# Performance work log

Measured on AMD Instinct MI355X. Metric: run time of the kernel, lower is better.

The kernel has to match this reference:

```python
import jax, jax.numpy as jnp
import numpy as np

B, N, D = 4, 1024, 512
H, DH = 8, 64
TC, AB = 512, 16
EPS = 1e-5
NEG = 1e6


def setup_inputs() -> dict:
    key = jax.random.key(0)
    ks = jax.random.split(key, 10)
    inp = {
        "x": jax.random.normal(ks[0], (B, N, D), jnp.float32),
        "time": jax.random.normal(ks[1], (B, 1, TC), jnp.float32),
        "attn_bias": jax.random.normal(ks[2], (B, AB, N, N), jnp.float32),
        "seq_mask": jnp.ones((B, N), jnp.float32),
        "gamma": jnp.ones((D,), jnp.float32),
        "Wt": jax.random.normal(ks[3], (2 * D, TC), jnp.float32) * 0.02,
        "bt": jnp.zeros((2 * D,), jnp.float32),
        "Wq": jax.random.normal(ks[4], (H * DH, D), jnp.float32) * 0.02,
        "Wkv": jax.random.normal(ks[5], (2 * H * DH, D), jnp.float32) * 0.02,
        "Wo": jax.random.normal(ks[6], (D, H * DH), jnp.float32) * 0.02,
        "Wb": jax.random.normal(ks[7], (H, AB), jnp.float32) * 0.02,
        "bb": jnp.zeros((H,), jnp.float32),
    }
    return inp


def reference(x, time, attn_bias, seq_mask, gamma, Wt, bt, Wq, Wkv, Wo, Wb, bb):
    # context defaults to raw x BEFORE norm/FiLM/mask (faithful to source order)
    ctx = x
    # LayerNorm (beta buffer is zero)
    mu = jnp.mean(x, axis=-1, keepdims=True)
    var = jnp.mean(jnp.square(x - mu), axis=-1, keepdims=True)
    xn = (x - mu) * jax.lax.rsqrt(var + EPS) * gamma
    # FiLM time conditioning: SiLU -> Linear -> chunk
    t = jax.nn.silu(time) @ Wt.T + bt            # [B,1,2D]
    scale, shift = jnp.split(t, 2, axis=-1)
    xn = xn * (scale + 1.0) + shift
    # seq mask on queries' input
    xn = xn * seq_mask[..., None]
    # projections
    q = xn @ Wq.T                                 # [B,N,H*DH]
    kv = ctx @ Wkv.T                              # [B,N,2*H*DH]
    k, v = jnp.split(kv, 2, axis=-1)
    to_heads = lambda t: t.reshape(B, N, H, DH).transpose(0, 2, 1, 3)
    q, k, v = to_heads(q), to_heads(k), to_heads(v)
    q = q * (DH ** -0.5)
    sim = jnp.einsum('bhid,bhjd->bhij', q, k)     # [B,H,N,N]
    # learned projection of attn_bias channels -> heads
    bias = jnp.einsum('baij,ha->bhij', attn_bias, Wb) + bb[None, :, None, None]
    sim = sim + bias
    m = seq_mask[:, None, :, None] * seq_mask[:, None, None, :]  # [B,1,N,N]
    sim = sim - (1.0 - m) * NEG
    attn = jax.nn.softmax(sim, axis=-1)
    out = jnp.einsum('bhij,bhjd->bhid', attn, v)
    out = out.transpose(0, 2, 1, 3).reshape(B, N, H * DH)
    out = out @ Wo.T
    return out * seq_mask[..., None]
```

## Files before the change

kernel.cpp:

```cpp
#include <hip/hip_runtime.h>
#include <hip/hip_bf16.h>
#include <math.h>

#define B_  4
#define N_  1024
#define D_  512
#define H_  8
#define DH_ 64
#define TC_ 512
#define AB_ 16
#define EPS_ 1e-5f
#define NEG_ 1e6f

typedef _Float16 half8v __attribute__((ext_vector_type(8)));
typedef _Float16 half4v __attribute__((ext_vector_type(4)));
typedef float floatx4 __attribute__((ext_vector_type(4)));

__global__ void film_kernel(const float* __restrict__ time_in,
                            const float* __restrict__ Wt,
                            const float* __restrict__ bt,
                            float* __restrict__ film) {
    int idx = blockIdx.x * blockDim.x + threadIdx.x;
    int b = idx >> 10;
    int c = idx & 1023;
    const float* trow = time_in + b * TC_;
    const float* wrow = Wt + (size_t)c * TC_;
    float acc = bt[c];
    for (int j = 0; j < TC_; ++j) {
        float tv = trow[j];
        float s = tv / (1.f + __expf(-tv));
        acc += s * wrow[j];
    }
    film[idx] = acc;
}

__global__ __launch_bounds__(256)
void cvt_f16_kernel(const float* __restrict__ in, _Float16* __restrict__ out,
                    int n4) {
    int i = blockIdx.x * blockDim.x + threadIdx.x;
    if (i < n4) {
        float4 v = ((const float4*)in)[i];
        half4v o;
        o.x = (_Float16)v.x; o.y = (_Float16)v.y;
        o.z = (_Float16)v.z; o.w = (_Float16)v.w;
        ((half4v*)out)[i] = o;
    }
}

__global__ __launch_bounds__(256)
void ln_film_kernel(const float* __restrict__ x,
                    const float* __restrict__ gamma,
                    const float* __restrict__ film,
                    const float* __restrict__ seq_mask,
                    _Float16* __restrict__ xnh) {
    int row = blockIdx.x;
    int b = row >> 10;
    int t = threadIdx.x;
    const float* xr = x + (size_t)row * D_;
    float v0 = xr[t];
    float v1 = xr[t + 256];
    float s = v0 + v1;
    float sq = v0 * v0 + v1 * v1;
    int lane = t & 63, wave = t >> 6;
    #pragma unroll
    for (int off = 32; off; off >>= 1) {
        s  += __shfl_down(s, off);
        sq += __shfl_down(sq, off);
    }
    __shared__ float rs[4], rq[4];
    if (lane == 0) { rs[wave] = s; rq[wave] = sq; }
    __syncthreads();
    float mu  = (rs[0] + rs[1] + rs[2] + rs[3]) * (1.f / D_);
    float ex2 = (rq[0] + rq[1] + rq[2] + rq[3]) * (1.f / D_);
    float var = ex2 - mu * mu;
    float rstd = rsqrtf(var + EPS_);
    float mrow = seq_mask[row];
    const float* scale = film + (size_t)b * 2 * D_;
    const float* shift = scale + D_;
    {
        int d = t;
        float val = (v0 - mu) * rstd * gamma[d];
        val = val * (scale[d] + 1.f) + shift[d];
        xnh[(size_t)row * D_ + d] = (_Float16)(val * mrow);
    }
    {
        int d = t + 256;
        float val = (v1 - mu) * rstd * gamma[d];
        val = val * (scale[d] + 1.f) + shift[d];
        xnh[(size_t)row * D_ + d] = (_Float16)(val * mrow);
    }
}

#define LDK 40
__global__ __launch_bounds__(256)
void gemm_mfma_f16(const _Float16* __restrict__ A,
                   const _Float16* __restrict__ Bt,
                   float* __restrict__ C,
                   int M, int Nn, int K) {
    __shared__ _Float16 As[128 * LDK];
    __shared__ _Float16 Bs[128 * LDK];
    int t = threadIdx.x;
    int wave = t >> 6, lane = t & 63;
    int quad = lane >> 4, l16 = lane & 15;
    int m0 = blockIdx.y * 128, n0 = blockIdx.x * 128;
    int wm = (wave >> 1) * 64, wn = (wave & 1) * 64;

    floatx4 acc[4][4];
    #pragma unroll
    for (int i = 0; i < 4; ++i)
        #pragma unroll
        for (int j = 0; j < 4; ++j)
            acc[i][j] = (floatx4){0.f, 0.f, 0.f, 0.f};

    int row0 = t >> 2;
    int seg0 = (t & 3) * 8;

    for (int k0 = 0; k0 < K; k0 += 32) {
        half8v a0 = *(const half8v*)(A  + (size_t)(m0 + row0)      * K + k0 + seg0);
        half8v a1 = *(const half8v*)(A  + (size_t)(m0 + row0 + 64) * K + k0 + seg0);
        half8v b0 = *(const half8v*)(Bt + (size_t)(n0 + row0)      * K + k0 + seg0);
        half8v b1 = *(const half8v*)(Bt + (size_t)(n0 + row0 + 64) * K + k0 + seg0);
        __syncthreads();
        *(half8v*)(As + row0 * LDK + seg0)        = a0;
        *(half8v*)(As + (row0 + 64) * LDK + seg0) = a1;
        *(half8v*)(Bs + row0 * LDK + seg0)        = b0;
        *(half8v*)(Bs + (row0 + 64) * LDK + seg0) = b1;
        __syncthreads();

        half8v af[4], bf[4];
        #pragma unroll
        for (int i = 0; i < 4; ++i)
            af[i] = *(half8v*)(As + (wm + i * 16 + l16) * LDK + quad * 8);
        #pragma unroll
        for (int j = 0; j < 4; ++j)
            bf[j] = *(half8v*)(Bs + (wn + j * 16 + l16) * LDK + quad * 8);
        #pragma unroll
        for (int i = 0; i < 4; ++i)
            #pragma unroll
            for (int j = 0; j < 4; ++j)
                acc[i][j] = __builtin_amdgcn_mfma_f32_16x16x32_f16(
                    af[i], bf[j], acc[i][j], 0, 0, 0);
    }

    #pragma unroll
    for (int i = 0; i < 4; ++i)
        #pragma unroll
        for (int j = 0; j < 4; ++j)
            #pragma unroll
            for (int r = 0; r < 4; ++r) {
                int grow = m0 + wm + i * 16 + quad * 4 + r;
                int gcol = n0 + wn + j * 16 + l16;
                C[(size_t)grow * Nn + gcol] = acc[i][j][r];
            }
}

__global__ __launch_bounds__(256)
void bias_proj_kernel(const float* __restrict__ ab,
                      const float* __restrict__ seq_mask,
                      const float* __restrict__ Wb,
                      const float* __restrict__ bb,
                      __hip_bfloat16* __restrict__ pb) {
    __shared__ float wbs[8][16];
    __shared__ float bbs[8];
    int blk = blockIdx.x;
    int b = blk >> 10;
    int i = blk & 1023;
    int t = threadIdx.x;
    if (t < 128) wbs[t >> 4][t & 15] = Wb[t];
    if (t < 8)   bbs[t] = bb[t];
    __syncthreads();

    float accx[8], accy[8], accz[8], accw[8];
    #pragma unroll
    for (int h = 0; h < 8; ++h) { accx[h] = accy[h] = accz[h] = accw[h] = bbs[h]; }

    const float* base = ab + ((size_t)(b * AB_) * N_ + i) * N_ + t * 4;
    #pragma unroll
    for (int a = 0; a < AB_; ++a) {
        float4 v = *(const float4*)(base + (size_t)a * N_ * N_);
        #pragma unroll
        for (int h = 0; h < 8; ++h) {
            float w = wbs[h][a];
            accx[h] += v.x * w;
            accy[h] += v.y * w;
            accz[h] += v.z * w;
            accw[h] += v.w * w;
        }
    }
    float mq = seq_mask[blk];
    float4 mk = *(const float4*)(seq_mask + b * N_ + t * 4);
    float px = (1.f - mq * mk.x) * NEG_;
    float py = (1.f - mq * mk.y) * NEG_;
    float pz = (1.f - mq * mk.z) * NEG_;
    float pw = (1.f - mq * mk.w) * NEG_;

    #pragma unroll
    for (int h = 0; h < 8; ++h) {
        __hip_bfloat16 tmp[4];
        tmp[0] = __float2bfloat16(accx[h] - px);
        tmp[1] = __float2bfloat16(accy[h] - py);
        tmp[2] = __float2bfloat16(accz[h] - pz);
        tmp[3] = __float2bfloat16(accw[h] - pw);
        size_t off = (((size_t)(b * 8 + h) * N_) + i) * N_ + t * 4;
        *(ushort4*)(pb + off) = *(ushort4*)tmp;
    }
}

#define LDF 72
#define LDP 72
#define LDV 68
__global__ __launch_bounds__(256, 4)
void flash_mfma_kernel(const float* __restrict__ q,
                       const float* __restrict__ kv,
                       const __hip_bfloat16* __restrict__ pb,
                       const float* __restrict__ seq_mask,
                       _Float16* __restrict__ atth) {
    __shared__ _Float16 Qs[64 * LDF];
    __shared__ _Float16 Ks[64 * LDF];
    __shared__ _Float16 Ps[64 * LDP];
    __shared__ _Float16 Vt[64 * LDV];

    int z  = blockIdx.x;
    int qt = z & 15;
    int h  = (z >> 4) & 7;
    int b  = z >> 7;
    int i0 = qt * 64;
    int t  = threadIdx.x;
    int wave = t >> 6, lane = t & 63;
    int quad = lane >> 4, l16 = lane & 15;
    int strip = wave * 16;

    const float* qbase = q + ((size_t)(b * N_ + i0)) * 512 + h * 64;
    #pragma unroll
    for (int l = 0; l < 4; ++l) {
        int idx = l * 256 + t;
        int r = idx >> 4, c4 = (idx & 15) * 4;
        float4 v = *(const float4*)(qbase + (size_t)r * 512 + c4);
        half4v o;
        o.x = (_Float16)(v.x * 0.125f);
        o.y = (_Float16)(v.y * 0.125f);
        o.z = (_Float16)(v.z * 0.125f);
        o.w = (_Float16)(v.w * 0.125f);
        *(half4v*)&Qs[r * LDF + c4] = o;
    }
    __syncthreads();
    half8v qf[2];
    qf[0] = *(half8v*)&Qs[(strip + l16) * LDF + quad * 8];
    qf[1] = *(half8v*)&Qs[(strip + l16) * LDF + 32 + quad * 8];

    float m_r[4], l_r[4];
    floatx4 acco[4];
    #pragma unroll
    for (int r = 0; r < 4; ++r) { m_r[r] = -1e30f; l_r[r] = 0.f; }
    #pragma unroll
    for (int tile = 0; tile < 4; ++tile)
        acco[tile] = (floatx4){0.f, 0.f, 0.f, 0.f};

    const float* kvbase = kv + (size_t)b * N_ * 1024 + h * 64;
    const __hip_bfloat16* pbb =
        pb + ((size_t)((b * 8 + h) * N_) + i0 + strip + quad * 4) * N_;

    for (int jt = 0; jt < 16; ++jt) {
        int j0 = jt * 64;
        float4 kreg[4], vreg[4];
        #pragma unroll
        for (int l = 0; l < 4; ++l) {
            int idx = l * 256 + t;
            int r = idx >> 4, c4 = (idx & 15) * 4;
            const float* p = kvbase + (size_t)(j0 + r) * 1024 + c4;
            kreg[l] = *(const float4*)p;
            vreg[l] = *(const float4*)(p + 512);
        }
        floatx4 accs[4];
        #pragma unroll
        for (int tile = 0; tile < 4; ++tile)
            #pragma unroll
            for (int r = 0; r < 4; ++r)
                accs[tile][r] = __bfloat162float(
                    pbb[(size_t)r * N_ + j0 + tile * 16 + l16]);

        __syncthreads();
        #pragma unroll
        for (int l = 0; l < 4; ++l) {
            int idx = l * 256 + t;
            int r = idx >> 4, c4 = (idx & 15) * 4;
            half4v kh;
            kh.x = (_Float16)kreg[l].x;
            kh.y = (_Float16)kreg[l].y;
            kh.z = (_Float16)kreg[l].z;
            kh.w = (_Float16)kreg[l].w;
            *(half4v*)&Ks[r * LDF + c4] = kh;
            Vt[(c4 + 0) * LDV + r] = (_Float16)vreg[l].x;
            Vt[(c4 + 1) * LDV + r] = (_Float16)vreg[l].y;
            Vt[(c4 + 2) * LDV + r] = (_Float16)vreg[l].z;
            Vt[(c4 + 3) * LDV + r] = (_Float16)vreg[l].w;
        }
        __syncthreads();

        #pragma unroll
        for (int c = 0; c < 2; ++c)
            #pragma unroll
            for (int tile = 0; tile < 4; ++tile) {
                half8v kf = *(half8v*)&Ks[(tile * 16 + l16) * LDF + c * 32 + quad * 8];
                accs[tile] = __builtin_amdgcn_mfma_f32_16x16x32_f16(
                    qf[c], kf, accs[tile], 0, 0, 0);
            }

        float rm[4];
        #pragma unroll
        for (int r = 0; r < 4; ++r)
            rm[r] = fmaxf(fmaxf(accs[0][r], accs[1][r]),
                          fmaxf(accs[2][r], accs[3][r]));
        #pragma unroll
        for (int off = 1; off < 16; off <<= 1)
            #pragma unroll
            for (int r = 0; r < 4; ++r)
                rm[r] = fmaxf(rm[r], __shfl_xor(rm[r], off));
        float alpha[4], rsum[4], pv[4][4];
        #pragma unroll
        for (int r = 0; r < 4; ++r) {
            float mn = fmaxf(m_r[r], rm[r]);
            alpha[r] = __expf(m_r[r] - mn);
            m_r[r] = mn;
            float s = 0.f;
            #pragma unroll
            for (int tile = 0; tile < 4; ++tile) {
                float e = __expf(accs[tile][r] - mn);
                pv[tile][r] = e;
                s += e;
            }
            rsum[r] = s;
        }
        #pragma unroll
        for (int off = 1; off < 16; off <<= 1)
            #pragma unroll
            for (int r = 0; r < 4; ++r)
                rsum[r] += __shfl_xor(rsum[r], off);
        #pragma unroll
        for (int r = 0; r < 4; ++r) {
            l_r[r] = l_r[r] * alpha[r] + rsum[r];
            #pragma unroll
            for (int tile = 0; tile < 4; ++tile) {
                acco[tile][r] *= alpha[r];
                Ps[(strip + quad * 4 + r) * LDP + tile * 16 + l16] =
                    (_Float16)pv[tile][r];
            }
        }
        __syncthreads();

        #pragma unroll
        for (int c = 0; c < 2; ++c) {
            half8v pf = *(half8v*)&Ps[(strip + l16) * LDP + c * 32 + quad * 8];
            #pragma unroll
            for (int tile = 0; tile < 4; ++tile) {
                union { half8v v8; half4v v4[2]; } vu;
                int vbase = (tile * 16 + l16) * LDV + c * 32 + quad * 8;
                vu.v4[0] = *(half4v*)&Vt[vbase];
                vu.v4[1] = *(half4v*)&Vt[vbase + 4];
                acco[tile] = __builtin_amdgcn_mfma_f32_16x16x32_f16(
                    pf, vu.v8, acco[tile], 0, 0, 0);
            }
        }
    }

    #pragma unroll
    for (int r = 0; r < 4; ++r) {
        int row = i0 + strip + quad * 4 + r;
        float msk = seq_mask[b * N_ + row];
        float inv = msk / l_r[r];
        _Float16* ob = atth + ((size_t)(b * N_ + row)) * 512 + h * 64;
        #pragma unroll
        for (int tile = 0; tile < 4; ++tile)
            ob[tile * 16 + l16] = (_Float16)(acco[tile][r] * inv);
    }
}

extern "C" void kernel_launch(void* const* d_in, const int* in_sizes, int n_in,
                              void* d_out, int out_size, void* d_ws, size_t ws_size,
                              hipStream_t stream) {
    const float* x         = (const float*)d_in[0];
    const float* time_in   = (const float*)d_in[1];
    const float* attn_bias = (const float*)d_in[2];
    const float* seq_mask  = (const float*)d_in[3];
    const float* gamma     = (const float*)d_in[4];
    const float* Wt        = (const float*)d_in[5];
    const float* bt        = (const float*)d_in[6];
    const float* Wq        = (const float*)d_in[7];
    const float* Wkv       = (const float*)d_in[8];
    const float* Wo        = (const float*)d_in[9];
    const float* Wb        = (const float*)d_in[10];
    const float* bb        = (const float*)d_in[11];
    float* out = (float*)d_out;

    char* ws = (char*)d_ws;
    const size_t KB = 1024, MB = 1024 * 1024;
    float*     film = (float*)ws;
    _Float16*  xnh  = (_Float16*)(ws + 16 * KB);
    _Float16*  xh   = (_Float16*)(ws + 16 * KB + 4 * MB);
    _Float16*  Wqh  = (_Float16*)(ws + 16 * KB + 8 * MB);
    _Float16*  Wkvh = (_Float16*)(ws + 16 * KB + 8 * MB + 512 * KB);
    _Float16*  Woh  = (_Float16*)(ws + 16 * KB + 9 * MB + 512 * KB);
    float*     qb   = (float*)(ws + 16 * KB + 10 * MB);
    float*     kvb  = (float*)(ws + 16 * KB + 18 * MB);
    _Float16*  atth = (_Float16*)(ws + 16 * KB + 34 * MB);
    __hip_bfloat16* pb = (__hip_bfloat16*)(ws + 16 * KB + 38 * MB);

    film_kernel<<<16, 256, 0, stream>>>(time_in, Wt, bt, film);
    ln_film_kernel<<<4096, 256, 0, stream>>>(x, gamma, film, seq_mask, xnh);
    cvt_f16_kernel<<<2048, 256, 0, stream>>>(x, xh, 4096 * 512 / 4);
    cvt_f16_kernel<<<256, 256, 0, stream>>>(Wq, Wqh, 512 * 512 / 4);
    cvt_f16_kernel<<<512, 256, 0, stream>>>(Wkv, Wkvh, 1024 * 512 / 4);
    cvt_f16_kernel<<<256, 256, 0, stream>>>(Wo, Woh, 512 * 512 / 4);

    dim3 gq(512 / 128, 4096 / 128);
    gemm_mfma_f16<<<gq, 256, 0, stream>>>(xnh, Wqh, qb, 4096, 512, 512);
    dim3 gkv(1024 / 128, 4096 / 128);
    gemm_mfma_f16<<<gkv, 256, 0, stream>>>(xh, Wkvh, kvb, 4096, 1024, 512);

    bias_proj_kernel<<<4096, 256, 0, stream>>>(attn_bias, seq_mask, Wb, bb, pb);
    flash_mfma_kernel<<<512, 256, 0, stream>>>(qb, kvb, pb, seq_mask, atth);

    dim3 go(512 / 128, 4096 / 128);
    gemm_mfma_f16<<<go, 256, 0, stream>>>(atth, Woh, out, 4096, 512, 512);
}
```

Baseline: 532.3 us.

## Emit fp16 Q/K/V-transposed from fused projection and double-buffer flash attention tiles

The Q and KV projections are merged into one launch that writes fp16 Q, fp16 K and a transposed fp16 V (computed as Wv·x^T). The Q scale is folded into the Wq conversion. The flash kernel loads these directly and drops its in-kernel fp32→fp16 conversion and scattered V transpose. It double-buffers K/V in LDS with register prefetch and prefetches the bias row, removing one barrier per tile, and raises MFMA priority with s_setprio. The FiLM kernel is parallelised with a wave per output and shuffle reductions. Together these cut global traffic and sync overhead, at the cost of more LDS per block and dropping the occupancy hint.

Measured after the change: 473.3 us. 1.12x faster.

```diff
diff --git a/kernel.cpp b/kernel.cpp
--- a/kernel.cpp
+++ b/kernel.cpp
@@ -16,33 +16,42 @@
 typedef _Float16 half4v __attribute__((ext_vector_type(4)));
 typedef float floatx4 __attribute__((ext_vector_type(4)));
 
-__global__ void film_kernel(const float* __restrict__ time_in,
-                            const float* __restrict__ Wt,
-                            const float* __restrict__ bt,
-                            float* __restrict__ film) {
-    int idx = blockIdx.x * blockDim.x + threadIdx.x;
-    int b = idx >> 10;
-    int c = idx & 1023;
+__global__ __launch_bounds__(256)
+void film_kernel(const float* __restrict__ time_in,
+                 const float* __restrict__ Wt,
+                 const float* __restrict__ bt,
+                 float* __restrict__ film) {
+    __shared__ float st[TC_];
+    int b = blockIdx.x >> 8;
+    int cblk = blockIdx.x & 255;
     const float* trow = time_in + b * TC_;
+    for (int j = threadIdx.x; j < TC_; j += 256) {
+        float tv = trow[j];
+        st[j] = tv / (1.f + __expf(-tv));
+    }
+    __syncthreads();
+    int wave = threadIdx.x >> 6, lane = threadIdx.x & 63;
+    int c = cblk * 4 + wave;
     const float* wrow = Wt + (size_t)c * TC_;
-    float acc = bt[c];
-    for (int j = 0; j < TC_; ++j) {
-        float tv = trow[j];
-        float s = tv / (1.f + __expf(-tv));
-        acc += s * wrow[j];
-    }
-    film[idx] = acc;
+    float acc = 0.f;
+    #pragma unroll
+    for (int j0 = 0; j0 < TC_; j0 += 64)
+        acc += st[j0 + lane] * wrow[j0 + lane];
+    #pragma unroll
+    for (int off = 32; off; off >>= 1)
+        acc += __shfl_down(acc, off);
+    if (lane == 0) film[b * 2 * D_ + c] = acc + bt[c];
 }
 
 __global__ __launch_bounds__(256)
 void cvt_f16_kernel(const float* __restrict__ in, _Float16* __restrict__ out,
-                    int n4) {
+                    int n4, float scale) {
     int i = blockIdx.x * blockDim.x + threadIdx.x;
     if (i < n4) {
         float4 v = ((const float4*)in)[i];
         half4v o;
-        o.x = (_Float16)v.x; o.y = (_Float16)v.y;
-        o.z = (_Float16)v.z; o.w = (_Float16)v.w;
+        o.x = (_Float16)(v.x * scale); o.y = (_Float16)(v.y * scale);
+        o.z = (_Float16)(v.z * scale); o.w = (_Float16)(v.w * scale);
         ((half4v*)out)[i] = o;
     }
 }
@@ -92,17 +101,17 @@
 }
 
 #define LDK 40
-__global__ __launch_bounds__(256)
-void gemm_mfma_f16(const _Float16* __restrict__ A,
-                   const _Float16* __restrict__ Bt,
-                   float* __restrict__ C,
-                   int M, int Nn, int K) {
-    __shared__ _Float16 As[128 * LDK];
-    __shared__ _Float16 Bs[128 * LDK];
+template <typename OUTT>
+__device__ __forceinline__
+void gemm_tile(const _Float16* __restrict__ A,
+               const _Float16* __restrict__ Bt,
+               OUTT* __restrict__ C,
+               int M, int Nn, int K, int bx, int by,
+               _Float16* As, _Float16* Bs) {
     int t = threadIdx.x;
     int wave = t >> 6, lane = t & 63;
     int quad = lane >> 4, l16 = lane & 15;
-    int m0 = blockIdx.y * 128, n0 = blockIdx.x * 128;
+    int m0 = by * 128, n0 = bx * 128;
     int wm = (wave >> 1) * 64, wn = (wave & 1) * 64;
 
     floatx4 acc[4][4];
@@ -150,8 +159,40 @@
             for (int r = 0; r < 4; ++r) {
                 int grow = m0 + wm + i * 16 + quad * 4 + r;
                 int gcol = n0 + wn + j * 16 + l16;
-                C[(size_t)grow * Nn + gcol] = acc[i][j][r];
-            }
+                C[(size_t)grow * Nn + gcol] = (OUTT)acc[i][j][r];
+            }
+}
+
+__global__ __launch_bounds__(256)
+void proj3_kernel(const _Float16* __restrict__ xnh,
+                  const _Float16* __restrict__ xh,
+                  const _Float16* __restrict__ Wqh,
+                  const _Float16* __restrict__ Wkvh,
+                  _Float16* __restrict__ qh,
+                  _Float16* __restrict__ kh,
+                  _Float16* __restrict__ vth) {
+    __shared__ _Float16 As[128 * LDK];
+    __shared__ _Float16 Bs[128 * LDK];
+    int z = blockIdx.x;
+    if (z < 128) {
+        gemm_tile<_Float16>(xnh, Wqh, qh, 4096, 512, 512, z & 3, z >> 2, As, Bs);
+    } else if (z < 256) {
+        int y = z - 128;
+        gemm_tile<_Float16>(xh, Wkvh, kh, 4096, 512, 512, y & 3, y >> 2, As, Bs);
+    } else {
+        int y = z - 256;
+        gemm_tile<_Float16>(Wkvh + 512 * 512, xh, vth, 512, 4096, 512,
+                            y & 31, y >> 5, As, Bs);
+    }
+}
+
+__global__ __launch_bounds__(256)
+void gemm_f32_kernel(const _Float16* __restrict__ A,
+                     const _Float16* __restrict__ Bt,
+                     float* __restrict__ C, int M, int Nn, int K) {
+    __shared__ _Float16 As[128 * LDK];
+    __shared__ _Float16 Bs[128 * LDK];
+    gemm_tile<float>(A, Bt, C, M, Nn, K, blockIdx.x, blockIdx.y, As, Bs);
 }
 
 __global__ __launch_bounds__(256)
@@ -208,17 +249,17 @@
 
 #define LDF 72
 #define LDP 72
-#define LDV 68
-__global__ __launch_bounds__(256, 4)
-void flash_mfma_kernel(const float* __restrict__ q,
-                       const float* __restrict__ kv,
+#define LDV 72
+__global__ __launch_bounds__(256)
+void flash_mfma_kernel(const _Float16* __restrict__ qh,
+                       const _Float16* __restrict__ kh,
+                       const _Float16* __restrict__ vth,
                        const __hip_bfloat16* __restrict__ pb,
                        const float* __restrict__ seq_mask,
                        _Float16* __restrict__ atth) {
-    __shared__ _Float16 Qs[64 * LDF];
-    __shared__ _Float16 Ks[64 * LDF];
+    __shared__ _Float16 Ks[2][64 * LDF];
+    __shared__ _Float16 Vt[2][64 * LDV];
     __shared__ _Float16 Ps[64 * LDP];
-    __shared__ _Float16 Vt[64 * LDV];
 
     int z  = blockIdx.x;
     int qt = z & 15;
@@ -230,81 +271,92 @@
     int quad = lane >> 4, l16 = lane & 15;
     int strip = wave * 16;
 
-    const float* qbase = q + ((size_t)(b * N_ + i0)) * 512 + h * 64;
-    #pragma unroll
-    for (int l = 0; l < 4; ++l) {
-        int idx = l * 256 + t;
-        int r = idx >> 4, c4 = (idx & 15) * 4;
-        float4 v = *(const float4*)(qbase + (size_t)r * 512 + c4);
-        half4v o;
-        o.x = (_Float16)(v.x * 0.125f);
-        o.y = (_Float16)(v.y * 0.125f);
-        o.z = (_Float16)(v.z * 0.125f);
-        o.w = (_Float16)(v.w * 0.125f);
-        *(half4v*)&Qs[r * LDF + c4] = o;
-    }
-    __syncthreads();
+    const _Float16* qbase =
+        qh + ((size_t)(b * N_ + i0 + strip + l16)) * 512 + h * 64;
     half8v qf[2];
-    qf[0] = *(half8v*)&Qs[(strip + l16) * LDF + quad * 8];
-    qf[1] = *(half8v*)&Qs[(strip + l16) * LDF + 32 + quad * 8];
+    qf[0] = *(const half8v*)(qbase + quad * 8);
+    qf[1] = *(const half8v*)(qbase + 32 + quad * 8);
+
+    const _Float16* kb0 = kh + (size_t)(b * N_) * 512 + h * 64;
+    const _Float16* vb0 = vth + (size_t)(h * 64) * 4096 + b * N_;
+    int sr = t >> 3;
+    int c8 = (t & 7) * 8;
+
+    half8v kr[2], vr[2];
+    #pragma unroll
+    for (int l = 0; l < 2; ++l) {
+        int r = l * 32 + sr;
+        kr[l] = *(const half8v*)(kb0 + (size_t)r * 512 + c8);
+        vr[l] = *(const half8v*)(vb0 + (size_t)r * 4096 + c8);
+    }
+
+    const __hip_bfloat16* pbb =
+        pb + ((size_t)((b * 8 + h) * N_) + i0 + strip + quad * 4) * N_;
+    unsigned short pbr[16];
+    #pragma unroll
+    for (int tl = 0; tl < 4; ++tl)
+        #pragma unroll
+        for (int r = 0; r < 4; ++r)
+            pbr[tl * 4 + r] =
+                *(const unsigned short*)(pbb + (size_t)r * N_ + tl * 16 + l16);
 
     float m_r[4], l_r[4];
     floatx4 acco[4];
     #pragma unroll
     for (int r = 0; r < 4; ++r) { m_r[r] = -1e30f; l_r[r] = 0.f; }
     #pragma unroll
-    for (int tile = 0; tile < 4; ++tile)
-        acco[tile] = (floatx4){0.f, 0.f, 0.f, 0.f};
-
-    const float* kvbase = kv + (size_t)b * N_ * 1024 + h * 64;
-    const __hip_bfloat16* pbb =
-        pb + ((size_t)((b * 8 + h) * N_) + i0 + strip + quad * 4) * N_;
+    for (int tl = 0; tl < 4; ++tl)
+        acco[tl] = (floatx4){0.f, 0.f, 0.f, 0.f};
 
     for (int jt = 0; jt < 16; ++jt) {
-        int j0 = jt * 64;
-        float4 kreg[4], vreg[4];
-        #pragma unroll
-        for (int l = 0; l < 4; ++l) {
-            int idx = l * 256 + t;
-            int r = idx >> 4, c4 = (idx & 15) * 4;
-            const float* p = kvbase + (size_t)(j0 + r) * 1024 + c4;
-            kreg[l] = *(const float4*)p;
-            vreg[l] = *(const float4*)(p + 512);
-        }
+        int cur = jt & 1;
+        _Float16* Ksc = Ks[cur];
+        _Float16* Vtc = Vt[cur];
+        #pragma unroll
+        for (int l = 0; l < 2; ++l) {
+            int r = l * 32 + sr;
+            *(half8v*)(Ksc + r * LDF + c8) = kr[l];
+            *(half8v*)(Vtc + r * LDV + c8) = vr[l];
+        }
+        __syncthreads();
+
+        if (jt < 15) {
+            int j0n = (jt + 1) * 64;
+            #pragma unroll
+            for (int l = 0; l < 2; ++l) {
+                int r = l * 32 + sr;
+                kr[l] = *(const half8v*)(kb0 + (size_t)(j0n + r) * 512 + c8);
+                vr[l] = *(const half8v*)(vb0 + (size_t)r * 4096 + j0n + c8);
+            }
+        }
+
         floatx4 accs[4];
         #pragma unroll
-        for (int tile = 0; tile < 4; ++tile)
+        for (int tl = 0; tl < 4; ++tl)
             #pragma unroll
             for (int r = 0; r < 4; ++r)
-                accs[tile][r] = __bfloat162float(
-                    pbb[(size_t)r * N_ + j0 + tile * 16 + l16]);
-
-        __syncthreads();
-        #pragma unroll
-        for (int l = 0; l < 4; ++l) {
-            int idx = l * 256 + t;
-            int r = idx >> 4, c4 = (idx & 15) * 4;
-            half4v kh;
-            kh.x = (_Float16)kreg[l].x;
-            kh.y = (_Float16)kreg[l].y;
-            kh.z = (_Float16)kreg[l].z;
-            kh.w = (_Float16)kreg[l].w;
-            *(half4v*)&Ks[r * LDF + c4] = kh;
-            Vt[(c4 + 0) * LDV + r] = (_Float16)vreg[l].x;
-            Vt[(c4 + 1) * LDV + r] = (_Float16)vreg[l].y;
-            Vt[(c4 + 2) * LDV + r] = (_Float16)vreg[l].z;
-            Vt[(c4 + 3) * LDV + r] = (_Float16)vreg[l].w;
-        }
-        __syncthreads();
-
+                accs[tl][r] = __uint_as_float((unsigned)pbr[tl * 4 + r] << 16);
+
+        if (jt < 15) {
+            int j0n = (jt + 1) * 64;
+            #pragma unroll
+            for (int tl = 0; tl < 4; ++tl)
+                #pragma unroll
+                for (int r = 0; r < 4; ++r)
+                    pbr[tl * 4 + r] = *(const unsigned short*)
+                        (pbb + (size_t)r * N_ + j0n + tl * 16 + l16);
+        }
+
+        __builtin_amdgcn_s_setprio(1);
         #pragma unroll
         for (int c = 0; c < 2; ++c)
             #pragma unroll
-            for (int tile = 0; tile < 4; ++tile) {
-                half8v kf = *(half8v*)&Ks[(tile * 16 + l16) * LDF + c * 32 + quad * 8];
-                accs[tile] = __builtin_amdgcn_mfma_f32_16x16x32_f16(
-                    qf[c], kf, accs[tile], 0, 0, 0);
-            }
+            for (int tl = 0; tl < 4; ++tl) {
+                half8v kf = *(half8v*)(Ksc + (tl * 16 + l16) * LDF + c * 32 + quad * 8);
+                accs[tl] = __builtin_amdgcn_mfma_f32_16x16x32_f16(
+                    qf[c], kf, accs[tl], 0, 0, 0);
+            }
+        __builtin_amdgcn_s_setprio(0);
 
         float rm[4];
         #pragma unroll
@@ -324,9 +376,9 @@
             m_r[r] = mn;
             float s = 0.f;
             #pragma unroll
-            for (int tile = 0; tile < 4; ++tile) {
-                float e = __expf(accs[tile][r] - mn);
-                pv[tile][r] = e;
+            for (int tl = 0; tl < 4; ++tl) {
+                float e = __expf(accs[tl][r] - mn);
+                pv[tl][r] = e;
                 s += e;
             }
             rsum[r] = s;
@@ -340,27 +392,25 @@
         for (int r = 0; r < 4; ++r) {
             l_r[r] = l_r[r] * alpha[r] + rsum[r];
             #pragma unroll
-            for (int tile = 0; tile < 4; ++tile) {
-                acco[tile][r] *= alpha[r];
-                Ps[(strip + quad * 4 + r) * LDP + tile * 16 + l16] =
-                    (_Float16)pv[tile][r];
-            }
-        }
-        __syncthreads();
-
+            for (int tl = 0; tl < 4; ++tl) {
+                acco[tl][r] *= alpha[r];
+                Ps[(strip + quad * 4 + r) * LDP + tl * 16 + l16] =
+                    (_Float16)pv[tl][r];
+            }
+        }
+
+        __builtin_amdgcn_s_setprio(1);
         #pragma unroll
         for (int c = 0; c < 2; ++c) {
-            half8v pf = *(half8v*)&Ps[(strip + l16) * LDP + c * 32 + quad * 8];
-            #pragma unroll
-            for (int tile = 0; tile < 4; ++tile) {
-                union { half8v v8; half4v v4[2]; } vu;
-                int vbase = (tile * 16 + l16) * LDV + c * 32 + quad * 8;
-                vu.v4[0] = *(half4v*)&Vt[vbase];
-                vu.v4[1] = *(half4v*)&Vt[vbase + 4];
-                acco[tile] = __builtin_amdgcn_mfma_f32_16x16x32_f16(
-                    pf, vu.v8, acco[tile], 0, 0, 0);
-            }
-        }
+            half8v pf = *(half8v*)(Ps + (strip + l16) * LDP + c * 32 + quad * 8);
+            #pragma unroll
+            for (int tl = 0; tl < 4; ++tl) {
+                half8v vf = *(half8v*)(Vtc + (tl * 16 + l16) * LDV + c * 32 + quad * 8);
+                acco[tl] = __builtin_amdgcn_mfma_f32_16x16x32_f16(
+                    pf, vf, acco[tl], 0, 0, 0);
+            }
+        }
+        __builtin_amdgcn_s_setprio(0);
     }
 
     #pragma unroll
@@ -370,8 +420,8 @@
         float inv = msk / l_r[r];
         _Float16* ob = atth + ((size_t)(b * N_ + row)) * 512 + h * 64;
         #pragma unroll
-        for (int tile = 0; tile < 4; ++tile)
-            ob[tile * 16 + l16] = (_Float16)(acco[tile][r] * inv);
+        for (int tl = 0; tl < 4; ++tl)
+            ob[tl * 16 + l16] = (_Float16)(acco[tl][r] * inv);
     }
 }
 
@@ -400,26 +450,24 @@
     _Float16*  Wqh  = (_Float16*)(ws + 16 * KB + 8 * MB);
     _Float16*  Wkvh = (_Float16*)(ws + 16 * KB + 8 * MB + 512 * KB);
     _Float16*  Woh  = (_Float16*)(ws + 16 * KB + 9 * MB + 512 * KB);
-    float*     qb   = (float*)(ws + 16 * KB + 10 * MB);
-    float*     kvb  = (float*)(ws + 16 * KB + 18 * MB);
-    _Float16*  atth = (_Float16*)(ws + 16 * KB + 34 * MB);
-    __hip_bfloat16* pb = (__hip_bfloat16*)(ws + 16 * KB + 38 * MB);
-
-    film_kernel<<<16, 256, 0, stream>>>(time_in, Wt, bt, film);
+    _Float16*  qh   = (_Float16*)(ws + 16 * KB + 10 * MB);
+    _Float16*  kh   = (_Float16*)(ws + 16 * KB + 14 * MB);
+    _Float16*  vth  = (_Float16*)(ws + 16 * KB + 18 * MB);
+    _Float16*  atth = (_Float16*)(ws + 16 * KB + 22 * MB);
+    __hip_bfloat16* pb = (__hip_bfloat16*)(ws + 16 * KB + 26 * MB);
+
+    film_kernel<<<1024, 256, 0, stream>>>(time_in, Wt, bt, film);
     ln_film_kernel<<<4096, 256, 0, stream>>>(x, gamma, film, seq_mask, xnh);
-    cvt_f16_kernel<<<2048, 256, 0, stream>>>(x, xh, 4096 * 512 / 4);
-    cvt_f16_kernel<<<256, 256, 0, stream>>>(Wq, Wqh, 512 * 512 / 4);
-    cvt_f16_kernel<<<512, 256, 0, stream>>>(Wkv, Wkvh, 1024 * 512 / 4);
-    cvt_f16_kernel<<<256, 256, 0, stream>>>(Wo, Woh, 512 * 512 / 4);
-
-    dim3 gq(512 / 128, 4096 / 128);
-    gemm_mfma_f16<<<gq, 256, 0, stream>>>(xnh, Wqh, qb, 4096, 512, 512);
-    dim3 gkv(1024 / 128, 4096 / 128);
-    gemm_mfma_f16<<<gkv, 256, 0, stream>>>(xh, Wkvh, kvb, 4096, 1024, 512);
+    cvt_f16_kernel<<<2048, 256, 0, stream>>>(x, xh, 4096 * 512 / 4, 1.f);
+    cvt_f16_kernel<<<256, 256, 0, stream>>>(Wq, Wqh, 512 * 512 / 4, 0.125f);
+    cvt_f16_kernel<<<512, 256, 0, stream>>>(Wkv, Wkvh, 1024 * 512 / 4, 1.f);
+    cvt_f16_kernel<<<256, 256, 0, stream>>>(Wo, Woh, 512 * 512 / 4, 1.f);
+
+    proj3_kernel<<<384, 256, 0, stream>>>(xnh, xh, Wqh, Wkvh, qh, kh, vth);
 
     bias_proj_kernel<<<4096, 256, 0, stream>>>(attn_bias, seq_mask, Wb, bb, pb);
-    flash_mfma_kernel<<<512, 256, 0, stream>>>(qb, kvb, pb, seq_mask, atth);
+    flash_mfma_kernel<<<512, 256, 0, stream>>>(qh, kh, vth, pb, seq_mask, atth);
 
     dim3 go(512 / 128, 4096 / 128);
-    gemm_mfma_f16<<<go, 256, 0, stream>>>(atth, Woh, out, 4096, 512, 512);
-}
+    gemm_f32_kernel<<<go, 256, 0, stream>>>(atth, Woh, out, 4096, 512, 512);
+}
```
